# Performance work log

Measured on AMD Instinct MI355X. Metric: run time of the kernel, lower is better.

## Reference

```python
import jax, jax.numpy as jnp
import numpy as np

C = 512; HEADS = 8; WH = 16; WW = 16; SH = 8; SW = 8; VCAP = 256; MLP = 2048


def _ln(x, g, b, eps=1e-5):
    m = x.mean(-1, keepdims=True)
    v = ((x - m) ** 2).mean(-1, keepdims=True)
    return (x - m) / jnp.sqrt(v + eps) * g + b


def setup_inputs() -> dict:
    key = jax.random.key(0)
    ks = jax.random.split(key, 12)
    P = 64; NV = 2048
    s = C ** -0.5
    d = {
        "patch_tokens": jax.random.normal(ks[0], (P * P, C), jnp.float32),
        "voxel_tokens": jax.random.normal(ks[1], (NV, C), jnp.float32),
        "ln1_g": jnp.ones((C,), jnp.float32), "ln1_b": jnp.zeros((C,), jnp.float32),
        "wq": jax.random.normal(ks[2], (C, C), jnp.float32) * s, "bq": jnp.zeros((C,), jnp.float32),
        "wk": jax.random.normal(ks[3], (C, C), jnp.float32) * s, "bk": jnp.zeros((C,), jnp.float32),
        "wv": jax.random.normal(ks[4], (C, C), jnp.float32) * s, "bv": jnp.zeros((C,), jnp.float32),
        "wo": jax.random.normal(ks[5], (C, C), jnp.float32) * s, "bo": jnp.zeros((C,), jnp.float32),
        "ln2_g": jnp.ones((C,), jnp.float32), "ln2_b": jnp.zeros((C,), jnp.float32),
        "w1": jax.random.normal(ks[6], (C, MLP), jnp.float32) * s, "b1": jnp.zeros((MLP,), jnp.float32),
        "w2": jax.random.normal(ks[7], (MLP, C), jnp.float32) * (MLP ** -0.5), "b2": jnp.zeros((C,), jnp.float32),
        "voxel_patch_y": jax.random.randint(ks[8], (NV,), 0, P),
        "voxel_patch_x": jax.random.randint(ks[9], (NV,), 0, P),
        "patch_h": P, "patch_w": P,
    }
    return d


def reference(patch_tokens, voxel_tokens, ln1_g, ln1_b, wq, bq, wk, bk, wv, bv,
              wo, bo, ln2_g, ln2_b, w1, b1, w2, b2,
              voxel_patch_y, voxel_patch_x, patch_h, patch_w):
    D = C // HEADS
    scale = D ** -0.5
    A = WH * WW  # window area (patch slots per window)
    grid = patch_tokens.reshape(patch_h, patch_w, C)

    # --- static window geometry (patch_h/w are python ints) ---
    ys0 = np.arange(0, patch_h, SH); xs0 = np.arange(0, patch_w, SW)
    Y0, X0 = np.meshgrid(ys0, xs0, indexing="ij")
    y0 = Y0.reshape(-1); x0 = X0.reshape(-1)          # [NW]
    NW = y0.shape[0]
    iy = y0[:, None] + np.arange(WH)[None, :]          # [NW, WH]
    ix = x0[:, None] + np.arange(WW)[None, :]          # [NW, WW]
    pvalid = (iy < patch_h)[:, :, None] & (ix < patch_w)[:, None, :]  # [NW,WH,WW]
    giy = np.minimum(iy, patch_h - 1); gix = np.minimum(ix, patch_w - 1)
    gidx = (giy[:, :, None] * patch_w + gix[:, None, :]).reshape(-1)  # [NW*A]
    pvalid_flat = jnp.asarray(pvalid.reshape(NW, A))

    # --- gather patch windows (invalid = zeros, like new_zeros in torch) ---
    wp = grid[giy[:, :, None], gix[:, None, :]]        # [NW,WH,WW,C]
    wp = jnp.where(jnp.asarray(pvalid)[..., None], wp, 0.0).reshape(NW, A, C)

    # --- per-window voxel gather with fixed capacity VCAP ---
    vy = voxel_patch_y; vx = voxel_patch_x
    member = ((vy[None, :] >= y0[:, None]) & (vy[None, :] < y0[:, None] + WH) &
              (vx[None, :] >= x0[:, None]) & (vx[None, :] < x0[:, None] + WW))  # [NW,NV]
    order = jnp.argsort(jnp.logical_not(member), axis=1)[:, :VCAP]     # members first
    vvalid = jnp.take_along_axis(member, order, axis=1)                # [NW,VCAP]
    wvox = voxel_tokens[order] * vvalid[..., None]                     # [NW,VCAP,C]

    tokens = jnp.concatenate([wp, wvox], axis=1)                       # [NW,S,C]
    pad = jnp.concatenate([~pvalid_flat, ~vvalid], axis=1)             # True = padded key
    S = A + VCAP

    # --- pre-norm attention block (batched over windows) ---
    h = _ln(tokens, ln1_g, ln1_b)
    q = (h @ wq + bq).reshape(NW, S, HEADS, D)
    k = (h @ wk + bk).reshape(NW, S, HEADS, D)
    v = (h @ wv + bv).reshape(NW, S, HEADS, D)
    scores = jnp.einsum("nqhd,nkhd->nhqk", q * scale, k)
    scores = jnp.where(pad[:, None, None, :], -jnp.inf, scores)
    attn = jax.nn.softmax(scores, axis=-1)
    o = jnp.einsum("nhqk,nkhd->nqhd", attn, v).reshape(NW, S, C)
    x = tokens + (o @ wo + bo)
    x = x + (jax.nn.gelu(_ln(x, ln2_g, ln2_b) @ w1 + b1, approximate=False) @ w2 + b2)
    x = jnp.where(pad[..., None], 0.0, x)

    # --- overlap-add fold back with count normalization ---
    updated = x[:, :A].reshape(-1, C)                                  # [NW*A,C]
    w = pvalid_flat.reshape(-1).astype(patch_tokens.dtype)
    Ptot = patch_h * patch_w
    accum = jnp.zeros((Ptot, C), patch_tokens.dtype).at[gidx].add(updated * w[:, None])
    counts = jnp.zeros((Ptot,), patch_tokens.dtype).at[gidx].add(w)
    return accum / jnp.maximum(counts, 1.0)[:, None]
```

## Files before the change

kernel.cpp:

```cpp
#include <hip/hip_runtime.h>
#include <math.h>

using u16 = unsigned short;
using u32 = unsigned int;
using u64 = unsigned long long;
using bf16x8 = __attribute__((ext_vector_type(8))) short;
using f32x4  = __attribute__((ext_vector_type(4))) float;

#define C_DIM   512
#define HEADS   8
#define HDIM    64
#define P_DIM   64
#define A_TOK   256
#define VCAP    256
#define S_TOK   512
#define NWIN    64
#define NROW    32768
#define NPATCH  16384
#define NUNIQ   6144
#define MLP_DIM 2048
#define NV_TOT  2048
#define LOG2E   1.44269504088896f

__device__ __forceinline__ float bf2f(u16 b) { return __uint_as_float(((u32)b) << 16); }
__device__ __forceinline__ u16 f2bf(float f) {
    u32 u = __float_as_uint(f);
    return (u16)((u + 0x7fffu + ((u >> 16) & 1u)) >> 16);
}
__device__ __forceinline__ u32 cvtpk(float lo, float hi) {
    u32 r;
    asm("v_cvt_pk_bf16_f32 %0, %1, %2" : "=v"(r) : "v"(lo), "v"(hi));
    return r;
}
__device__ __forceinline__ float4 bf4f(ushort4 v) {
    return make_float4(bf2f(v.x), bf2f(v.y), bf2f(v.z), bf2f(v.w));
}
__device__ __forceinline__ float ldf(const void* p, size_t e, int isbf) {
    return isbf ? bf2f(((const u16*)p)[e]) : ((const float*)p)[e];
}
__device__ __forceinline__ float4 ld4(const void* p, size_t e, int isbf) {
    if (isbf) return bf4f(*(const ushort4*)((const u16*)p + e));
    return *(const float4*)((const float*)p + e);
}
__device__ __forceinline__ void gload16(const u16* g, u16* l) {
    __builtin_amdgcn_global_load_lds(
        (const __attribute__((address_space(1))) u32*)g,
        (__attribute__((address_space(3))) u32*)l, 16, 0, 0);
}
__device__ __forceinline__ float fast_gelu(float x) {
    float x2 = x * x;
    float z = x * (-2.3021083f - 0.10294323f * x2);
    float e = exp2f(z);
    return x * __builtin_amdgcn_rcpf(1.f + e);
}
__device__ __forceinline__ int self_detect(const u32* patch, int tid, int* sm)
{
    int cnt = 0;
    for (int i = tid; i < 4096; i += 256) {
        u32 w = patch[i];
        float a = fabsf(__uint_as_float((w & 0xffffu) << 16));
        if (a > 1e-8f && a < 1e4f) cnt++;
    }
    sm[tid] = cnt;
    __syncthreads();
    for (int o = 128; o; o >>= 1) { if (tid < o) sm[tid] += sm[tid + o]; __syncthreads(); }
    int r = (sm[0] > 2458) ? 1 : 0;
    __syncthreads();
    return r;
}

__global__ __launch_bounds__(256) void setup_kernel(
    const void* __restrict__ wq, const void* __restrict__ wk,
    const void* __restrict__ wv, const void* __restrict__ wo,
    const void* __restrict__ w1, const void* __restrict__ w2,
    const void* __restrict__ bq, const void* __restrict__ bk, const void* __restrict__ bv,
    const void* __restrict__ patch,
    const int* __restrict__ vy, const int* __restrict__ vx,
    u16* __restrict__ wqkvT, u16* __restrict__ woT,
    u16* __restrict__ w1T, u16* __restrict__ w2T,
    float* __restrict__ bqkv, u16* __restrict__ tokidx, unsigned char* __restrict__ validk,
    int* __restrict__ wcnt, int* __restrict__ flagp)
{
    __shared__ int sm[256];
    __shared__ u16 tile[32][33];
    int tx = threadIdx.x, ty = threadIdx.y;
    int tid = ty * 32 + tx;
    int isbf = self_detect((const u32*)patch, tid, sm);
    int bid = blockIdx.x;
    if (bid == 0 && tid == 0) *flagp = isbf;

    if (bid < 3072) {
        int id = bid;
        const void* in; u16* out; int K, N; float sc = 1.f;
        if (id < 256)       { in = wq; out = wqkvT;              K = 512;  N = 512;  sc = 0.125f * LOG2E; }
        else if (id < 512)  { id -= 256;  in = wk; out = wqkvT + 512 * 512;  K = 512;  N = 512; }
        else if (id < 768)  { id -= 512;  in = wv; out = wqkvT + 1024 * 512; K = 512;  N = 512; }
        else if (id < 1024) { id -= 768;  in = wo; out = woT;    K = 512;  N = 512; }
        else if (id < 2048) { id -= 1024; in = w1; out = w1T;    K = 512;  N = 2048; }
        else                { id -= 2048; in = w2; out = w2T;    K = 2048; N = 512; }
        int ntx = N >> 5;
        int n0 = (id % ntx) * 32, k0 = (id / ntx) * 32;
        #pragma unroll
        for (int i = 0; i < 4; i++)
            tile[ty + i * 8][tx] = f2bf(sc * ldf(in, (size_t)(k0 + ty + i * 8) * N + (n0 + tx), isbf));
        __syncthreads();
        #pragma unroll
        for (int i = 0; i < 4; i++)
            out[(size_t)(n0 + ty + i * 8) * K + (k0 + tx)] = tile[tx][ty + i * 8];
    } else if (bid < 3136) {
        if (tid < 64) {
            int n = bid - 3072, lane = tid;
            int y0 = (n >> 3) << 3, x0 = (n & 7) << 3;
            int count = 0;
            for (int base = 0; base < NV_TOT; base += 64) {
                int v = base + lane;
                int yy = vy[v], xx = vx[v];
                bool m = (yy >= y0) && (yy < y0 + 16) && (xx >= x0) && (xx < x0 + 16);
                u64 mask = __ballot(m);
                int pos = count + __popcll(mask & ((1ull << lane) - 1ull));
                if (m && pos < VCAP) tokidx[n * S_TOK + A_TOK + pos] = (u16)(4096 + v);
                count += __popcll(mask);
            }
            int cn = count < VCAP ? count : VCAP;
            for (int j = lane; j < VCAP; j += 64) {
                if (j >= cn) tokidx[n * S_TOK + A_TOK + j] = 0;
                validk[n * S_TOK + A_TOK + j] = (j < cn) ? 1 : 0;
            }
            for (int s = lane; s < A_TOK; s += 64) {
                int iy = ((n >> 3) << 3) + (s >> 4);
                int ix = ((n & 7) << 3) + (s & 15);
                bool val = (iy < P_DIM) && (ix < P_DIM);
                tokidx[n * S_TOK + s] = val ? (u16)(iy * P_DIM + ix) : 0;
                validk[n * S_TOK + s] = val ? 1 : 0;
            }
            if (lane == 0) wcnt[n] = cn;
        }
    } else {
        int t = (bid - 3136) * 256 + tid;
        if (t < 512)       bqkv[t] = 0.125f * LOG2E * ldf(bq, t, isbf);
        else if (t < 1024) bqkv[t] = ldf(bk, t - 512, isbf);
        else if (t < 1536) bqkv[t] = ldf(bv, t - 1024, isbf);
    }
}

__global__ __launch_bounds__(256) void ln1u_kernel(
    const void* __restrict__ patch, const void* __restrict__ vox,
    const void* __restrict__ g, const void* __restrict__ b,
    const int* __restrict__ flagp,
    u16* __restrict__ h)
{
    int isbf = *flagp;
    int r = blockIdx.x * 4 + (threadIdx.x >> 6);
    int lane = threadIdx.x & 63;
    const void* tok = (r < 4096) ? patch : vox;
    size_t base = (r < 4096) ? (size_t)r * C_DIM : (size_t)(r - 4096) * C_DIM;
    float4 xa = ld4(tok, base + lane * 4, isbf);
    float4 xb = ld4(tok, base + 256 + lane * 4, isbf);
    float sum = xa.x + xa.y + xa.z + xa.w + xb.x + xb.y + xb.z + xb.w;
    float sq  = xa.x * xa.x + xa.y * xa.y + xa.z * xa.z + xa.w * xa.w
              + xb.x * xb.x + xb.y * xb.y + xb.z * xb.z + xb.w * xb.w;
    #pragma unroll
    for (int off = 32; off; off >>= 1) {
        sum += __shfl_xor(sum, off, 64);
        sq  += __shfl_xor(sq,  off, 64);
    }
    float mean = sum * (1.f / C_DIM);
    float var  = fmaxf(sq * (1.f / C_DIM) - mean * mean, 0.f);
    float rstd = rsqrtf(var + 1e-5f);
    float4 ga = ld4(g, lane * 4, isbf);
    float4 gb = ld4(g, 256 + lane * 4, isbf);
    float4 ba = ld4(b, lane * 4, isbf);
    float4 bb = ld4(b, 256 + lane * 4, isbf);
    uint2 wa, wb;
    wa.x = cvtpk((xa.x - mean) * rstd * ga.x + ba.x, (xa.y - mean) * rstd * ga.y + ba.y);
    wa.y = cvtpk((xa.z - mean) * rstd * ga.z + ba.z, (xa.w - mean) * rstd * ga.w + ba.w);
    wb.x = cvtpk((xb.x - mean) * rstd * gb.x + bb.x, (xb.y - mean) * rstd * gb.y + bb.y);
    wb.y = cvtpk((xb.z - mean) * rstd * gb.z + bb.z, (xb.w - mean) * rstd * gb.w + bb.w);
    ((uint2*)(h + (size_t)r * C_DIM))[lane]      = wa;
    ((uint2*)(h + (size_t)r * C_DIM))[lane + 64] = wb;
}

__global__ __launch_bounds__(256) void ln2_kernel(
    const u16* __restrict__ x,
    const void* __restrict__ g, const void* __restrict__ b,
    const int* __restrict__ flagp,
    u16* __restrict__ h2)
{
    int isbf = *flagp;
    int r = blockIdx.x * 4 + (threadIdx.x >> 6);
    int lane = threadIdx.x & 63;
    const u16* src = x + (size_t)r * C_DIM;
    float4 xa = bf4f(((const ushort4*)src)[lane]);
    float4 xb = bf4f(((const ushort4*)src)[lane + 64]);
    float sum = xa.x + xa.y + xa.z + xa.w + xb.x + xb.y + xb.z + xb.w;
    float sq  = xa.x * xa.x + xa.y * xa.y + xa.z * xa.z + xa.w * xa.w
              + xb.x * xb.x + xb.y * xb.y + xb.z * xb.z + xb.w * xb.w;
    #pragma unroll
    for (int off = 32; off; off >>= 1) {
        sum += __shfl_xor(sum, off, 64);
        sq  += __shfl_xor(sq,  off, 64);
    }
    float mean = sum * (1.f / C_DIM);
    float var  = fmaxf(sq * (1.f / C_DIM) - mean * mean, 0.f);
    float rstd = rsqrtf(var + 1e-5f);
    float4 ga = ld4(g, lane * 4, isbf);
    float4 gb = ld4(g, 256 + lane * 4, isbf);
    float4 ba = ld4(b, lane * 4, isbf);
    float4 bb = ld4(b, 256 + lane * 4, isbf);
    uint2 wa, wb;
    wa.x = cvtpk((xa.x - mean) * rstd * ga.x + ba.x, (xa.y - mean) * rstd * ga.y + ba.y);
    wa.y = cvtpk((xa.z - mean) * rstd * ga.z + ba.z, (xa.w - mean) * rstd * ga.w + ba.w);
    wb.x = cvtpk((xb.x - mean) * rstd * gb.x + bb.x, (xb.y - mean) * rstd * gb.y + bb.y);
    wb.y = cvtpk((xb.z - mean) * rstd * gb.z + bb.z, (xb.w - mean) * rstd * gb.w + bb.w);
    ((uint2*)(h2 + (size_t)r * C_DIM))[lane]      = wa;
    ((uint2*)(h2 + (size_t)r * C_DIM))[lane + 64] = wb;
}

#define GF_GELU      2
#define GF_RES_BF16  8
#define GF_RES_PATCH 16
#define GF_QKV       32
#define GF_PATCHM    64

template<int FLAGS>
__global__ __launch_bounds__(256) void gemm_kernel(
    const u16* __restrict__ A, const u16* __restrict__ BT,
    const void* __restrict__ bias,
    void* __restrict__ Cout, void* __restrict__ Cout2, void* __restrict__ Cout3,
    const void* __restrict__ resv,
    const int* __restrict__ flagp,
    int M, int N, int K, int ldc)
{
    __shared__ u16 smem[2 * 128 * 64];
    int tid = threadIdx.x;
    int nt, mt;
    int gx = gridDim.x, gy = gridDim.y;
    if ((gy & 7) == 0) {
        int L = blockIdx.x + gx * blockIdx.y;
        int c = L & 7, s = L >> 3;
        mt = c * (gy >> 3) + s / gx;
        nt = s % gx;
    } else { nt = blockIdx.x; mt = blockIdx.y; }
    int m0 = mt << 7, n0 = nt << 7;
    int region = (FLAGS & GF_QKV) ? (nt >> 2) : 0;
    if constexpr (FLAGS & GF_QKV) {
        if (region == 0 && m0 >= 4096) return;
    }
    if constexpr (FLAGS & GF_PATCHM) {
        int n = mt >> 1;
        if ((n >> 3) == 7 && (mt & 1) == 1) return;
    }
    int isbf = 0;
    if constexpr ((FLAGS & (GF_RES_PATCH)) || (!(FLAGS & GF_QKV))) isbf = *flagp;
    int w = tid >> 6, lane = tid & 63;
    int wr = (w >> 1) * 64, wc = (w & 1) * 64;
    int l16 = lane & 15, quad = lane >> 4;
    u16* As = smem;
    u16* Bs = smem + 8192;
    bool vtb = (FLAGS & GF_QKV) && (region == 2);

    f32x4 acc[4][4];
    #pragma unroll
    for (int i = 0; i < 4; i++)
        #pragma unroll
        for (int j = 0; j < 4; j++) { acc[i][j][0] = 0.f; acc[i][j][1] = 0.f; acc[i][j][2] = 0.f; acc[i][j][3] = 0.f; }

    int swz = (l16 & 7);
    const u16* Xs = vtb ? Bs : As;
    const u16* Ys = vtb ? As : Bs;
    for (int k0 = 0; k0 < K; k0 += 64) {
        #pragma unroll
        for (int it = 0; it < 4; it++) {
            int c = (it * 4 + w) * 64 + lane;
            int row = c >> 3, phys = c & 7;
            int kc = phys ^ (row & 7);
            gload16(A  + (size_t)(m0 + row) * K + k0 + kc * 8, As + (size_t)c * 8);
            gload16(BT + (size_t)(n0 + row) * K + k0 + kc * 8, Bs + (size_t)c * 8);
        }
        __syncthreads();
        #pragma unroll
        for (int ks = 0; ks < 2; ks++) {
            bf16x8 a[4], b[4];
            #pragma unroll
            for (int i = 0; i < 4; i++) {
                int chunk = (ks * 4 + quad) ^ swz;
                a[i] = *(const bf16x8*)&Xs[(wr + i * 16 + l16) * 64 + chunk * 8];
            }
            #pragma unroll
            for (int j = 0; j < 4; j++) {
                int chunk = (ks * 4 + quad) ^ swz;
                b[j] = *(const bf16x8*)&Ys[(wc + j * 16 + l16) * 64 + chunk * 8];
            }
            #pragma unroll
            for (int i = 0; i < 4; i++)
                #pragma unroll
                for (int j = 0; j < 4; j++)
                    acc[i][j] = __builtin_amdgcn_mfma_f32_16x16x32_bf16(a[i], b[j], acc[i][j], 0, 0, 0);
        }
        __syncthreads();
    }

    u16* st = smem + w * 4096;
    #pragma unroll
    for (int i = 0; i < 4; i++) {
        #pragma unroll
        for (int j = 0; j < 4; j++) {
            int gcol = n0 + wc + j * 16 + l16;
            float bc = 0.f;
            if constexpr (FLAGS & GF_QKV) { if (!vtb) bc = ((const float*)bias)[gcol]; }
            else if (bias) bc = ldf(bias, gcol, isbf);
            float vv[4];
            #pragma unroll
            for (int r2 = 0; r2 < 4; r2++) {
                int lrow = wr + i * 16 + quad * 4 + r2;
                int grow = m0 + lrow;
                if (vtb) bc = ((const float*)bias)[n0 + lrow];
                float v = acc[i][j][r2] + bc;
                if constexpr (FLAGS & GF_GELU) v = fast_gelu(v);
                if constexpr (FLAGS & GF_RES_BF16) v += bf2f(((const u16*)resv)[(size_t)grow * N + gcol]);
                if constexpr (FLAGS & GF_RES_PATCH) {
                    int nn = grow >> 8, s = grow & 255;
                    int iy = ((nn >> 3) << 3) + (s >> 4);
                    int ix = ((nn & 7) << 3) + (s & 15);
                    if (iy < P_DIM && ix < P_DIM)
                        v += ldf(resv, (size_t)(iy * P_DIM + ix) * C_DIM + gcol, isbf);
                }
                vv[r2] = v;
            }
            u32 p01 = cvtpk(vv[0], vv[1]);
            u32 p23 = cvtpk(vv[2], vv[3]);
            int sb = (i * 16 + quad * 4) * 64 + j * 16 + l16;
            st[sb]       = (u16)p01;
            st[sb + 64]  = (u16)(p01 >> 16);
            st[sb + 128] = (u16)p23;
            st[sb + 192] = (u16)(p23 >> 16);
        }
    }
    asm volatile("" ::: "memory");
    u16* cdst; int cst;
    if constexpr (FLAGS & GF_QKV) {
        if (region == 0) {
            cst = 512;
            cdst = (u16*)Cout  + (size_t)(m0 + wr) * 512 + (n0 + wc);
        } else if (region == 1) {
            cst = 512;
            cdst = (u16*)Cout2 + (size_t)(m0 + wr) * 512 + (n0 - 512 + wc);
        } else {
            cst = NUNIQ;
            cdst = (u16*)Cout3 + (size_t)(n0 - 1024 + wr) * NUNIQ + (m0 + wc);
        }
    } else {
        cst = ldc;
        cdst = (u16*)Cout + (size_t)(m0 + wr) * ldc + (n0 + wc);
    }
    #pragma unroll
    for (int rr = 0; rr < 8; rr++) {
        int row = rr * 8 + (lane >> 3);
        uint4 val = *(const uint4*)&st[row * 64 + (lane & 7) * 8];
        *(uint4*)(cdst + (size_t)row * cst + (lane & 7) * 8) = val;
    }
}

__global__ __launch_bounds__(256) void expandv_kernel(
    const u16* __restrict__ vTU, const u16* __restrict__ tokidx,
    u16* __restrict__ vtt)
{
    int gid = blockIdx.x * 256 + threadIdx.x;
    int d = gid >> 12;
    int c = gid & 4095;
    int n = c >> 6, s0 = (c & 63) * 8;
    const u16* tp = tokidx + n * S_TOK + s0;
    ushort4 ta = *(const ushort4*)tp;
    ushort4 tb = *(const ushort4*)(tp + 4);
    const u16* vr = vTU + (size_t)d * NUNIQ;
    uint4 val;
    val.x = (u32)vr[ta.x] | ((u32)vr[ta.y] << 16);
    val.y = (u32)vr[ta.z] | ((u32)vr[ta.w] << 16);
    val.z = (u32)vr[tb.x] | ((u32)vr[tb.y] << 16);
    val.w = (u32)vr[tb.z] | ((u32)vr[tb.w] << 16);
    *(uint4*)(vtt + (size_t)d * NROW + n * S_TOK + s0) = val;
}

__global__ __launch_bounds__(256) void attn_kernel(
    const u16* __restrict__ q, const u16* __restrict__ kU, const u16* __restrict__ vtg,
    const u16* __restrict__ tokidx,
    const unsigned char* __restrict__ validk, const int* __restrict__ wcnt,
    u16* __restrict__ o)
{
    __shared__ u16 sK[64 * 64];
    __shared__ u16 sV[64 * 64];
    __shared__ u16 sP[4 * 64 * 64];
    int h = blockIdx.x, n = blockIdx.y;
    int tid = threadIdx.x;
    int w = tid >> 6, lane = tid & 63;
    int l16 = lane & 15, quad = lane >> 4;
    int swz = (l16 & 7);
    int cnt = wcnt[n];

    int rowA = tid >> 3;
    u16 tokA[8], tokB[8];
    #pragma unroll
    for (int t = 0; t < 8; t++) {
        tokA[t] = tokidx[n * S_TOK + t * 64 + rowA];
        tokB[t] = tokidx[n * S_TOK + t * 64 + 32 + rowA];
    }

    bf16x8 qf[4][2];
    #pragma unroll
    for (int i = 0; i < 4; i++)
        #pragma unroll
        for (int ks = 0; ks < 2; ks++) {
            int tok = tokidx[n * S_TOK + w * 64 + i * 16 + l16];
            int col = h * HDIM + ks * 32 + quad * 8;
            qf[i][ks] = *(const bf16x8*)(q + (size_t)tok * C_DIM + col);
        }

    f32x4 oacc[4][4];
    float lsum[4][4];
    #pragma unroll
    for (int i = 0; i < 4; i++)
        #pragma unroll
        for (int j = 0; j < 4; j++) {
            oacc[i][j][0] = 0.f; oacc[i][j][1] = 0.f; oacc[i][j][2] = 0.f; oacc[i][j][3] = 0.f;
            lsum[i][j] = 0.f;
        }

    for (int ktile = 0; ktile < 8; ktile++) {
        if (ktile >= 4 && cnt <= (ktile - 4) * 64) break;
        __syncthreads();
        #pragma unroll
        for (int it = 0; it < 2; it++) {
            int c = it * 256 + w * 64 + lane;
            int row = c >> 3, phys = c & 7;
            int kc = phys ^ (row & 7);
            int tok = (it == 0) ? tokA[ktile] : tokB[ktile];
            gload16(kU + (size_t)tok * C_DIM + h * HDIM + kc * 8, sK + (size_t)c * 8);
            gload16(vtg + (size_t)(h * HDIM + row) * (size_t)NROW + n * S_TOK + ktile * 64 + kc * 8,
                    sV + (size_t)c * 8);
        }
        __syncthreads();

        f32x4 sacc[4][4];
        #pragma unroll
        for (int i = 0; i < 4; i++)
            #pragma unroll
            for (int j = 0; j < 4; j++) { sacc[i][j][0] = 0.f; sacc[i][j][1] = 0.f; sacc[i][j][2] = 0.f; sacc[i][j][3] = 0.f; }
        #pragma unroll
        for (int ks = 0; ks < 2; ks++) {
            int chunk = (ks * 4 + quad) ^ swz;
            bf16x8 bfr[4];
            #pragma unroll
            for (int j = 0; j < 4; j++) bfr[j] = *(const bf16x8*)&sK[(j * 16 + l16) * 64 + chunk * 8];
            #pragma unroll
            for (int i = 0; i < 4; i++)
                #pragma unroll
                for (int j = 0; j < 4; j++)
                    sacc[i][j] = __builtin_amdgcn_mfma_f32_16x16x32_bf16(qf[i][ks], bfr[j], sacc[i][j], 0, 0, 0);
        }

        bool kvalid[4];
        #pragma unroll
        for (int j = 0; j < 4; j++)
            kvalid[j] = validk[n * S_TOK + ktile * 64 + j * 16 + l16] != 0;

        #pragma unroll
        for (int i = 0; i < 4; i++)
            #pragma unroll
            for (int r2 = 0; r2 < 4; r2++) {
                int prow = i * 16 + quad * 4 + r2;
                float pv[4];
                #pragma unroll
                for (int j = 0; j < 4; j++) {
                    pv[j] = kvalid[j] ? exp2f(sacc[i][j][r2]) : 0.f;
                    lsum[i][r2] += pv[j];
                }
                #pragma unroll
                for (int jp = 0; jp < 2; jp++) {
                    u32 pk = cvtpk(pv[2 * jp], pv[2 * jp + 1]);
                    int col0 = (2 * jp) * 16 + l16;
                    int col1 = col0 + 16;
                    int base_ = (w * 64 + prow) * 64;
                    sP[base_ + (((col0 >> 3) ^ (prow & 7)) << 3) + (col0 & 7)] = (u16)pk;
                    sP[base_ + (((col1 >> 3) ^ (prow & 7)) << 3) + (col1 & 7)] = (u16)(pk >> 16);
                }
            }
        asm volatile("" ::: "memory");
        #pragma unroll
        for (int ks = 0; ks < 2; ks++) {
            int chunk = (ks * 4 + quad) ^ swz;
            bf16x8 pa[4], vb[4];
            #pragma unroll
            for (int i = 0; i < 4; i++)   pa[i]  = *(const bf16x8*)&sP[(w * 64 + i * 16 + l16) * 64 + chunk * 8];
            #pragma unroll
            for (int jd = 0; jd < 4; jd++) vb[jd] = *(const bf16x8*)&sV[(jd * 16 + l16) * 64 + chunk * 8];
            #pragma unroll
            for (int i = 0; i < 4; i++)
                #pragma unroll
                for (int jd = 0; jd < 4; jd++)
                    oacc[i][jd] = __builtin_amdgcn_mfma_f32_16x16x32_bf16(pa[i], vb[jd], oacc[i][jd], 0, 0, 0);
        }
    }

    asm volatile("" ::: "memory");
    __syncthreads();
    u16* ost = sP + w * 4096;
    #pragma unroll
    for (int i = 0; i < 4; i++) {
        #pragma unroll
        for (int r2 = 0; r2 < 4; r2++) {
            float l = lsum[i][r2];
            #pragma unroll
            for (int off = 8; off; off >>= 1)
                l += __shfl_xor(l, off, 64);
            float inv = (l > 0.f) ? 1.f / l : 0.f;
            int ob_ = (i * 16 + quad * 4 + r2) * 64 + l16;
            u32 q01 = cvtpk(oacc[i][0][r2] * inv, oacc[i][1][r2] * inv);
            u32 q23 = cvtpk(oacc[i][2][r2] * inv, oacc[i][3][r2] * inv);
            ost[ob_]      = (u16)q01;
            ost[ob_ + 16] = (u16)(q01 >> 16);
            ost[ob_ + 32] = (u16)q23;
            ost[ob_ + 48] = (u16)(q23 >> 16);
        }
    }
    asm volatile("" ::: "memory");
    u16* obase = o + (size_t)(n * A_TOK + w * 64) * C_DIM + h * HDIM;
    #pragma unroll
    for (int rr = 0; rr < 8; rr++) {
        int row = rr * 8 + (lane >> 3);
        uint4 val = *(const uint4*)&ost[row * 64 + (lane & 7) * 8];
        *(uint4*)(obase + (size_t)row * C_DIM + (lane & 7) * 8) = val;
    }
}

__global__ __launch_bounds__(256) void gather_kernel(const u16* __restrict__ xf,
                                                     void* __restrict__ out,
                                                     const int* __restrict__ flagp)
{
    int isbf = *flagp;
    int gid = blockIdx.x * 256 + threadIdx.x;
    int p = gid >> 7, cv = gid & 127;
    int py = p >> 6, px = p & 63;
    float4 acc = make_float4(0.f, 0.f, 0.f, 0.f);
    int cnt = 0;
    #pragma unroll
    for (int dy = 0; dy < 2; dy++) {
        int y0 = ((py >> 3) - dy) << 3;
        if (y0 < 0) continue;
        #pragma unroll
        for (int dx = 0; dx < 2; dx++) {
            int x0 = ((px >> 3) - dx) << 3;
            if (x0 < 0) continue;
            int n = ((y0 >> 3) << 3) + (x0 >> 3);
            int s = (py - y0) * 16 + (px - x0);
            float4 t = bf4f(((const ushort4*)(xf + (size_t)(n * A_TOK + s) * C_DIM))[cv]);
            acc.x += t.x; acc.y += t.y; acc.z += t.z; acc.w += t.w;
            cnt++;
        }
    }
    float inv = 1.f / (float)cnt;
    acc.x *= inv; acc.y *= inv; acc.z *= inv; acc.w *= inv;
    if (isbf) {
        uint2 o;
        o.x = cvtpk(acc.x, acc.y);
        o.y = cvtpk(acc.z, acc.w);
        ((uint2*)out)[gid] = o;
    } else {
        ((float4*)out)[gid] = acc;
    }
}

extern "C" void kernel_launch(void* const* d_in, const int* in_sizes, int n_in,
                              void* d_out, int out_size, void* d_ws, size_t ws_size,
                              hipStream_t stream)
{
    const void* patch = d_in[0];
    const void* vox   = d_in[1];
    const void* ln1g  = d_in[2];
    const void* ln1b  = d_in[3];
    const void* wq = d_in[4];  const void* bq = d_in[5];
    const void* wk = d_in[6];  const void* bk = d_in[7];
    const void* wv = d_in[8];  const void* bv = d_in[9];
    const void* wo = d_in[10]; const void* bo = d_in[11];
    const void* ln2g = d_in[12];
    const void* ln2b = d_in[13];
    const void* w1 = d_in[14]; const void* b1 = d_in[15];
    const void* w2 = d_in[16]; const void* b2 = d_in[17];
    const int* vpy = (const int*)d_in[18];
    const int* vpx = (const int*)d_in[19];

    const size_t MB = 1ull << 20;
    char* ws = (char*)d_ws;
    if (ws_size < 128 * MB) return;

    u16*  hU    = (u16*)(ws + 0);
    u16*  kU    = (u16*)(ws + 6 * MB);
    u16*  vTU   = (u16*)(ws + 12 * MB);
    u16*  qU    = (u16*)(ws + 18 * MB);
    u16*  vtt   = (u16*)(ws + 22 * MB);
    u16*  tbuf  = (u16*)(ws + 0);
    u16*  obuf  = (u16*)(ws + 64 * MB);
    u16*  xfbuf = (u16*)(ws + 64 * MB);
    u16*  xbuf16 = (u16*)(ws + 80 * MB);
    u16*  h2buf = (u16*)(ws + 96 * MB);
    u16* wqkvT = (u16*)(ws + 112 * MB);
    u16* woT  = (u16*)(ws + 114 * MB);
    u16* w1T  = (u16*)(ws + 115 * MB);
    u16* w2T  = (u16*)(ws + 117 * MB);
    u16* tokidx = (u16*)(ws + 119 * MB);
    unsigned char* validk = (unsigned char*)(ws + 119 * MB + 64 * 1024);
    int* flagp = (int*)(ws + 119 * MB + 128 * 1024);
    float* bqkv = (float*)(ws + 119 * MB + 132 * 1024);
    int* wcnt = (int*)(ws + 119 * MB + 140 * 1024);

    setup_kernel<<<3142, dim3(32, 8), 0, stream>>>(wq, wk, wv, wo, w1, w2, bq, bk, bv,
        patch, vpy, vpx, wqkvT, woT, w1T, w2T, bqkv, tokidx, validk, wcnt, flagp);

    ln1u_kernel<<<NUNIQ / 4, 256, 0, stream>>>(patch, vox, ln1g, ln1b, flagp, hU);

    gemm_kernel<GF_QKV><<<dim3(12, NUNIQ / 128), 256, 0, stream>>>(hU, wqkvT, bqkv,
        qU, kU, vTU, nullptr, flagp, NUNIQ, 1536, 512, 512);

    expandv_kernel<<<(C_DIM * NROW / 8) / 256, 256, 0, stream>>>(vTU, tokidx, vtt);

    attn_kernel<<<dim3(HEADS, NWIN), 256, 0, stream>>>(qU, kU, vtt, tokidx, validk, wcnt, obuf);

    gemm_kernel<GF_RES_PATCH | GF_PATCHM><<<dim3(4, NPATCH / 128), 256, 0, stream>>>(obuf, woT, bo,
        xbuf16, nullptr, nullptr, patch, flagp, NPATCH, 512, 512, 512);

    ln2_kernel<<<NPATCH / 4, 256, 0, stream>>>(xbuf16, ln2g, ln2b, flagp, h2buf);

    gemm_kernel<GF_GELU | GF_PATCHM><<<dim3(16, NPATCH / 128), 256, 0, stream>>>(h2buf, w1T, b1,
        tbuf, nullptr, nullptr, nullptr, flagp, NPATCH, 2048, 512, 2048);
    gemm_kernel<GF_RES_BF16 | GF_PATCHM><<<dim3(4, NPATCH / 128), 256, 0, stream>>>(tbuf, w2T, b2,
        xfbuf, nullptr, nullptr, xbuf16, flagp, NPATCH, 512, 2048, 512);

    gather_kernel<<<(4096 * 128) / 256, 256, 0, stream>>>(xfbuf, d_out, flagp);
}
```

Baseline: 380.1 us.

## Load GEMM B operand and attention K/V fragments directly from global into registers

In the GEMM, only the X operand is staged through shared memory. The Y operand fragments are now loaded straight from global memory into registers, with the second k-half prefetched during the barrier. In attention, the K and V tiles are no longer staged in shared memory: each wave gathers its MFMA fragments directly from global, and the per-tile block barriers are removed. This trades LDS traffic and synchronisation for redundant, less coalesced global loads, since every wave re-reads the same K/V and B data through the cache.

Measured after the change: 464.1 us. 1.22x slower.

```diff
diff --git a/kernel.cpp b/kernel.cpp
--- a/kernel.cpp
+++ b/kernel.cpp
@@ -231,7 +231,7 @@
     const int* __restrict__ flagp,
     int M, int N, int K, int ldc)
 {
-    __shared__ u16 smem[2 * 128 * 64];
+    __shared__ u16 smem[4 * 4096];
     int tid = threadIdx.x;
     int nt, mt;
     int gx = gridDim.x, gy = gridDim.y;
@@ -255,10 +255,12 @@
     int w = tid >> 6, lane = tid & 63;
     int wr = (w >> 1) * 64, wc = (w & 1) * 64;
     int l16 = lane & 15, quad = lane >> 4;
-    u16* As = smem;
-    u16* Bs = smem + 8192;
     bool vtb = (FLAGS & GF_QKV) && (region == 2);
 
+    const u16* Xsrc = vtb ? BT : A;   int xbase = vtb ? n0 : m0;
+    const u16* Ysrc = vtb ? A  : BT;  int ybase = vtb ? m0 : n0;
+    const u16* ybp = Ysrc + (size_t)(ybase + wc + l16) * K + quad * 8;
+
     f32x4 acc[4][4];
     #pragma unroll
     for (int i = 0; i < 4; i++)
@@ -266,36 +268,45 @@
         for (int j = 0; j < 4; j++) { acc[i][j][0] = 0.f; acc[i][j][1] = 0.f; acc[i][j][2] = 0.f; acc[i][j][3] = 0.f; }
 
     int swz = (l16 & 7);
-    const u16* Xs = vtb ? Bs : As;
-    const u16* Ys = vtb ? As : Bs;
     for (int k0 = 0; k0 < K; k0 += 64) {
+        bf16x8 yb0[4], yb1[4];
+        #pragma unroll
+        for (int j = 0; j < 4; j++)
+            yb0[j] = *(const bf16x8*)(ybp + (size_t)j * 16 * K + k0);
         #pragma unroll
         for (int it = 0; it < 4; it++) {
             int c = (it * 4 + w) * 64 + lane;
             int row = c >> 3, phys = c & 7;
             int kc = phys ^ (row & 7);
-            gload16(A  + (size_t)(m0 + row) * K + k0 + kc * 8, As + (size_t)c * 8);
-            gload16(BT + (size_t)(n0 + row) * K + k0 + kc * 8, Bs + (size_t)c * 8);
+            gload16(Xsrc + (size_t)(xbase + row) * K + k0 + kc * 8, smem + (size_t)c * 8);
         }
         __syncthreads();
         #pragma unroll
-        for (int ks = 0; ks < 2; ks++) {
-            bf16x8 a[4], b[4];
-            #pragma unroll
-            for (int i = 0; i < 4; i++) {
-                int chunk = (ks * 4 + quad) ^ swz;
-                a[i] = *(const bf16x8*)&Xs[(wr + i * 16 + l16) * 64 + chunk * 8];
-            }
-            #pragma unroll
-            for (int j = 0; j < 4; j++) {
-                int chunk = (ks * 4 + quad) ^ swz;
-                b[j] = *(const bf16x8*)&Ys[(wc + j * 16 + l16) * 64 + chunk * 8];
-            }
+        for (int j = 0; j < 4; j++)
+            yb1[j] = *(const bf16x8*)(ybp + (size_t)j * 16 * K + k0 + 32);
+        {
+            int chunk = quad ^ swz;
+            bf16x8 a[4];
+            #pragma unroll
+            for (int i = 0; i < 4; i++)
+                a[i] = *(const bf16x8*)&smem[(wr + i * 16 + l16) * 64 + chunk * 8];
             #pragma unroll
             for (int i = 0; i < 4; i++)
                 #pragma unroll
                 for (int j = 0; j < 4; j++)
-                    acc[i][j] = __builtin_amdgcn_mfma_f32_16x16x32_bf16(a[i], b[j], acc[i][j], 0, 0, 0);
+                    acc[i][j] = __builtin_amdgcn_mfma_f32_16x16x32_bf16(a[i], yb0[j], acc[i][j], 0, 0, 0);
+        }
+        {
+            int chunk = (4 + quad) ^ swz;
+            bf16x8 a[4];
+            #pragma unroll
+            for (int i = 0; i < 4; i++)
+                a[i] = *(const bf16x8*)&smem[(wr + i * 16 + l16) * 64 + chunk * 8];
+            #pragma unroll
+            for (int i = 0; i < 4; i++)
+                #pragma unroll
+                for (int j = 0; j < 4; j++)
+                    acc[i][j] = __builtin_amdgcn_mfma_f32_16x16x32_bf16(a[i], yb1[j], acc[i][j], 0, 0, 0);
         }
         __syncthreads();
     }
@@ -387,8 +398,6 @@
     const unsigned char* __restrict__ validk, const int* __restrict__ wcnt,
     u16* __restrict__ o)
 {
-    __shared__ u16 sK[64 * 64];
-    __shared__ u16 sV[64 * 64];
     __shared__ u16 sP[4 * 64 * 64];
     int h = blockIdx.x, n = blockIdx.y;
     int tid = threadIdx.x;
@@ -397,14 +406,6 @@
     int swz = (l16 & 7);
     int cnt = wcnt[n];
 
-    int rowA = tid >> 3;
-    u16 tokA[8], tokB[8];
-    #pragma unroll
-    for (int t = 0; t < 8; t++) {
-        tokA[t] = tokidx[n * S_TOK + t * 64 + rowA];
-        tokB[t] = tokidx[n * S_TOK + t * 64 + 32 + rowA];
-    }
-
     bf16x8 qf[4][2];
     #pragma unroll
     for (int i = 0; i < 4; i++)
@@ -427,18 +428,15 @@
 
     for (int ktile = 0; ktile < 8; ktile++) {
         if (ktile >= 4 && cnt <= (ktile - 4) * 64) break;
-        __syncthreads();
-        #pragma unroll
-        for (int it = 0; it < 2; it++) {
-            int c = it * 256 + w * 64 + lane;
-            int row = c >> 3, phys = c & 7;
-            int kc = phys ^ (row & 7);
-            int tok = (it == 0) ? tokA[ktile] : tokB[ktile];
-            gload16(kU + (size_t)tok * C_DIM + h * HDIM + kc * 8, sK + (size_t)c * 8);
-            gload16(vtg + (size_t)(h * HDIM + row) * (size_t)NROW + n * S_TOK + ktile * 64 + kc * 8,
-                    sV + (size_t)c * 8);
-        }
-        __syncthreads();
+
+        int ktok[4];
+        bool kvalid[4];
+        #pragma unroll
+        for (int j = 0; j < 4; j++) {
+            int s = n * S_TOK + ktile * 64 + j * 16 + l16;
+            ktok[j] = tokidx[s];
+            kvalid[j] = validk[s] != 0;
+        }
 
         f32x4 sacc[4][4];
         #pragma unroll
@@ -447,21 +445,16 @@
             for (int j = 0; j < 4; j++) { sacc[i][j][0] = 0.f; sacc[i][j][1] = 0.f; sacc[i][j][2] = 0.f; sacc[i][j][3] = 0.f; }
         #pragma unroll
         for (int ks = 0; ks < 2; ks++) {
-            int chunk = (ks * 4 + quad) ^ swz;
             bf16x8 bfr[4];
             #pragma unroll
-            for (int j = 0; j < 4; j++) bfr[j] = *(const bf16x8*)&sK[(j * 16 + l16) * 64 + chunk * 8];
+            for (int j = 0; j < 4; j++)
+                bfr[j] = *(const bf16x8*)(kU + (size_t)ktok[j] * C_DIM + h * HDIM + ks * 32 + quad * 8);
             #pragma unroll
             for (int i = 0; i < 4; i++)
                 #pragma unroll
                 for (int j = 0; j < 4; j++)
                     sacc[i][j] = __builtin_amdgcn_mfma_f32_16x16x32_bf16(qf[i][ks], bfr[j], sacc[i][j], 0, 0, 0);
         }
-
-        bool kvalid[4];
-        #pragma unroll
-        for (int j = 0; j < 4; j++)
-            kvalid[j] = validk[n * S_TOK + ktile * 64 + j * 16 + l16] != 0;
 
         #pragma unroll
         for (int i = 0; i < 4; i++)
@@ -490,19 +483,21 @@
             int chunk = (ks * 4 + quad) ^ swz;
             bf16x8 pa[4], vb[4];
             #pragma unroll
-            for (int i = 0; i < 4; i++)   pa[i]  = *(const bf16x8*)&sP[(w * 64 + i * 16 + l16) * 64 + chunk * 8];
-            #pragma unroll
-            for (int jd = 0; jd < 4; jd++) vb[jd] = *(const bf16x8*)&sV[(jd * 16 + l16) * 64 + chunk * 8];
+            for (int i = 0; i < 4; i++)
+                pa[i] = *(const bf16x8*)&sP[(w * 64 + i * 16 + l16) * 64 + chunk * 8];
+            #pragma unroll
+            for (int jd = 0; jd < 4; jd++)
+                vb[jd] = *(const bf16x8*)(vtg + (size_t)(h * HDIM + jd * 16 + l16) * NROW
+                                          + n * S_TOK + ktile * 64 + (ks * 4 + quad) * 8);
             #pragma unroll
             for (int i = 0; i < 4; i++)
                 #pragma unroll
                 for (int jd = 0; jd < 4; jd++)
                     oacc[i][jd] = __builtin_amdgcn_mfma_f32_16x16x32_bf16(pa[i], vb[jd], oacc[i][jd], 0, 0, 0);
         }
-    }
-
-    asm volatile("" ::: "memory");
-    __syncthreads();
+        asm volatile("" ::: "memory");
+    }
+
     u16* ost = sP + w * 4096;
     #pragma unroll
     for (int i = 0; i < 4; i++) {
```
